# Kernel tuning notes

Measured on AMD Instinct MI355X. Metric: run time of the kernel, lower is better.

## Reference

```python
import jax, jax.numpy as jnp
import numpy as np

D = 16      # chem_dims
K = 16      # hard-coded k in Atom_embedding
N = 81920   # query points
M = 20000   # atoms
EPS = 1e-5  # BatchNorm eps


def _knn_idx(x, y, x_batch, y_batch, k, chunk=1024):
    """Block-diagonal kNN: indices of k nearest atoms in y for each point in x,
    restricted to matching batch ids (mirrors pykeops diagonal_ranges)."""
    n = x.shape[0]
    nch = n // chunk
    yb = y_batch[None, :]

    def f(args):
        xc, xbc = args                                            # [chunk,3], [chunk]
        d = jnp.sum((xc[:, None, :] - y[None, :, :]) ** 2, -1)    # [chunk, M]
        d = jnp.where(xbc[:, None] == yb, d, jnp.inf)
        _, idx = jax.lax.top_k(-d, k)                             # k smallest dists
        return idx

    idx = jax.lax.map(f, (x.reshape(nch, chunk, 3), x_batch.reshape(nch, chunk)))
    return idx.reshape(n, k)


def _bn_eval(h, gamma, beta, mean, var):
    # eval-mode BatchNorm1d over last dim
    return (h - mean) * (gamma * jax.lax.rsqrt(var + EPS)) + beta


def setup_inputs() -> dict:
    key = jax.random.key(0)
    ks = jax.random.split(key, 12)
    inp = {
        "x": jax.random.uniform(ks[0], (N, 3), jnp.float32) * 10.0,
        "y": jax.random.uniform(ks[1], (M, 3), jnp.float32) * 10.0,
        "y_atomtypes": jax.random.normal(ks[2], (M, D), jnp.float32),
        "x_batch": jnp.zeros((N,), jnp.int32),
        "y_batch": jnp.zeros((M,), jnp.int32),
        "W1": jax.random.normal(ks[3], (D + 1, D), jnp.float32) * 0.1,
        "b1": jnp.zeros((D,), jnp.float32),
        "W2": jax.random.normal(ks[4], (D, D), jnp.float32) * 0.1,
        "b2": jnp.zeros((D,), jnp.float32),
        "W3": jax.random.normal(ks[5], (2 * D, D), jnp.float32) * 0.1,
        "b3": jnp.zeros((D,), jnp.float32),
        "bn1_g": jnp.ones((D,), jnp.float32),
        "bn1_b": jnp.zeros((D,), jnp.float32),
        "bn1_m": jax.random.normal(ks[6], (D,), jnp.float32) * 0.1,
        "bn1_v": jnp.ones((D,), jnp.float32),
        "bn2_g": jnp.ones((D,), jnp.float32),
        "bn2_b": jnp.zeros((D,), jnp.float32),
        "bn2_m": jax.random.normal(ks[7], (D,), jnp.float32) * 0.1,
        "bn2_v": jnp.ones((D,), jnp.float32),
    }
    return inp


def reference(x, y, y_atomtypes, x_batch, y_batch,
              W1, b1, W2, b2, W3, b3,
              bn1_g, bn1_b, bn1_m, bn1_v,
              bn2_g, bn2_b, bn2_m, bn2_v):
    idx = _knn_idx(x, y, x_batch, y_batch, K)            # [N, K] int32
    yk = y[idx]                                          # [N, K, 3]
    dists = jnp.sum((x[:, None, :] - yk) ** 2, -1)       # [N, K]
    feat = jnp.concatenate(
        [y_atomtypes[idx], (1.0 / dists)[..., None]], -1)  # [N, K, D+1]
    # dropout in eval mode == identity
    h = feat @ W1 + b1                                   # conv1
    h = _bn_eval(jax.nn.leaky_relu(h, 0.2), bn1_g, bn1_b, bn1_m, bn1_v)
    fx1 = jnp.sum(h, axis=1)                             # [N, D]
    h2 = h @ W2 + b2                                     # conv2
    h2 = _bn_eval(jax.nn.leaky_relu(h2, 0.2), bn2_g, bn2_b, bn2_m, bn2_v)
    fx2 = jnp.sum(h2, axis=1)                            # [N, D]
    out = jnp.concatenate([fx1, fx2], -1) @ W3 + b3      # conv3 -> [N, D]
    return out
```

## Files before the change

kernel.cpp:

```cpp
#include <hip/hip_runtime.h>

#define N_PTS 81920
#define M_PTS 20000
#define NC 14
#define NCELLS 2744
#define CELLW 0.7142857143f
#define INVCELL 1.4f
#define BIGF 3.0e38f
#define CAP_STAGE 264
#define PPC 16
#define WPB 4
#define MAX_TASKS 7880

__device__ __forceinline__ int clampi(int v, int lo, int hi) {
  return v < lo ? lo : (v > hi ? hi : v);
}
__device__ __forceinline__ int cell_coord(float p) {
  return clampi((int)(p * INVCELL), 0, NC - 1);
}
__device__ __forceinline__ float floorpack(float d) {
  return __uint_as_float(__float_as_uint(d) & 0xFFFF8000u);
}


__global__ void hist_both_kernel(const float* __restrict__ y, const float* __restrict__ x,
                                 int* __restrict__ ycnt, int* __restrict__ xcnt) {
  int i = blockIdx.x * blockDim.x + threadIdx.x;
  if (i < M_PTS) {
    int c = (cell_coord(y[3*i+2])*NC + cell_coord(y[3*i+1]))*NC + cell_coord(y[3*i]);
    atomicAdd(&ycnt[c], 1);
  } else {
    int j = i - M_PTS;
    if (j < N_PTS) {
      int c = (cell_coord(x[3*j+2])*NC + cell_coord(x[3*j+1]))*NC + cell_coord(x[3*j]);
      atomicAdd(&xcnt[c], 1);
    }
  }
}

__global__ void scan2_kernel(const int* __restrict__ ycnt, int* __restrict__ ystart, int* __restrict__ ycur,
                             const int* __restrict__ xcnt, int* __restrict__ xstart, int* __restrict__ xcur,
                             int* __restrict__ tasks, int* __restrict__ ntasks) {
  const int* cnt = (blockIdx.x == 0) ? ycnt : xcnt;
  int* start     = (blockIdx.x == 0) ? ystart : xstart;
  int* cursor    = (blockIdx.x == 0) ? ycur : xcur;
  __shared__ int tmp[1024];
  int tid = threadIdx.x;
  int chunk = (NCELLS + 1023) >> 10;
  int base = tid * chunk;
  int sum = 0;
  for (int k = 0; k < chunk; ++k) {
    int j = base + k;
    if (j < NCELLS) sum += cnt[j];
  }
  tmp[tid] = sum;
  __syncthreads();
  for (int off = 1; off < 1024; off <<= 1) {
    int v = (tid >= off) ? tmp[tid - off] : 0;
    __syncthreads();
    tmp[tid] += v;
    __syncthreads();
  }
  int run = tmp[tid] - sum;
  for (int k = 0; k < chunk; ++k) {
    int j = base + k;
    if (j < NCELLS) { start[j] = run; cursor[j] = run; run += cnt[j]; }
  }
  if (tid == 1023) start[NCELLS] = tmp[1023];

  if (blockIdx.x == 1) {
    int tsum = 0;
    for (int k = 0; k < chunk; ++k) {
      int j = base + k;
      if (j < NCELLS) tsum += (cnt[j] + PPC - 1) / PPC;
    }
    __syncthreads();
    tmp[tid] = tsum;
    __syncthreads();
    for (int off = 1; off < 1024; off <<= 1) {
      int v = (tid >= off) ? tmp[tid - off] : 0;
      __syncthreads();
      tmp[tid] += v;
      __syncthreads();
    }
    int trun = tmp[tid] - tsum;
    for (int k = 0; k < chunk; ++k) {
      int j = base + k;
      if (j < NCELLS) {
        int nch = (cnt[j] + PPC - 1) / PPC;
        for (int q2 = 0; q2 < nch; ++q2) tasks[trun++] = (q2 << 12) | j;
      }
    }
    if (tid == 1023) ntasks[0] = tmp[1023];
  }
}

__global__ void scatter_both_kernel(const float* __restrict__ y, const float* __restrict__ x,
                                    int* __restrict__ ycur, int* __restrict__ xcur,
                                    float4* __restrict__ ys4, int* __restrict__ xorder,
                                    float4* __restrict__ xs4, float4* __restrict__ y4) {
  int i = blockIdx.x * blockDim.x + threadIdx.x;
  if (i < M_PTS) {
    float px = y[3*i], py = y[3*i+1], pz = y[3*i+2];
    if (y4) y4[i] = make_float4(px, py, pz, 0.0f);
    int c = (cell_coord(pz)*NC + cell_coord(py))*NC + cell_coord(px);
    int pos = atomicAdd(&ycur[c], 1);
    ys4[pos] = make_float4(px, py, pz, __int_as_float(i));
  } else {
    int j = i - M_PTS;
    if (j < N_PTS) {
      float px = x[3*j], py = x[3*j+1], pz = x[3*j+2];
      int c = (cell_coord(pz)*NC + cell_coord(py))*NC + cell_coord(px);
      int pos = atomicAdd(&xcur[c], 1);
      xorder[pos] = j;
      if (xs4) xs4[pos] = make_float4(px, py, pz, __int_as_float(j));
    }
  }
}

__global__ void sortcell_kernel(float4* __restrict__ ys4, const int* __restrict__ ystart) {
  int c = blockIdx.x * blockDim.x + threadIdx.x;
  if (c >= NCELLS) return;
  int r0 = ystart[c], r1 = ystart[c+1];
  for (int i = r0 + 1; i < r1; ++i) {
    float4 v = ys4[i];
    int key = __float_as_int(v.w);
    int j = i - 1;
    while (j >= r0 && __float_as_int(ys4[j].w) > key) { ys4[j+1] = ys4[j]; --j; }
    ys4[j+1] = v;
  }
}

__device__ __forceinline__ void bitonic_sort16(float (&d)[16]) {
  #define CE(a,b) { float lo=fminf(d[a],d[b]); float hi=fmaxf(d[a],d[b]); d[a]=lo; d[b]=hi; }
  CE(0,8) CE(1,9) CE(2,10) CE(3,11) CE(4,12) CE(5,13) CE(6,14) CE(7,15)
  CE(0,4) CE(1,5) CE(2,6) CE(3,7) CE(8,12) CE(9,13) CE(10,14) CE(11,15)
  CE(0,2) CE(1,3) CE(4,6) CE(5,7) CE(8,10) CE(9,11) CE(12,14) CE(13,15)
  CE(0,1) CE(2,3) CE(4,5) CE(6,7) CE(8,9) CE(10,11) CE(12,13) CE(14,15)
  #undef CE
}

__device__ __forceinline__ void ins16(float (&s)[16], float k) {
  #pragma unroll
  for (int j = 15; j >= 1; --j) s[j] = fminf(fmaxf(s[j-1], k), s[j]);
  s[0] = fminf(s[0], k);
}

__global__ void __launch_bounds__(256) knn_cell_kernel(
    const float4* __restrict__ xs4,
    const float4* __restrict__ ys4, const int* __restrict__ ystart,
    const int* __restrict__ xstart,
    const int* __restrict__ tasks, const int* __restrict__ ntasks,
    unsigned short* __restrict__ pi)
{
  __shared__ float4 cand_all[WPB][CAP_STAGE];
  int wid = threadIdx.x >> 6;
  int tid = threadIdx.x & 63;
  int ti = blockIdx.x * WPB + wid;
  if (ti >= ntasks[0]) return;
  int task = tasks[ti];
  int c = task & 4095, chunk = task >> 12;
  int cbeg = xstart[c];
  int cend = xstart[c+1];
  int pbeg = cbeg + chunk*PPC;
  int pend = min(cend, pbeg + PPC);

  float4* cand = cand_all[wid];

  int ccx = c % NC, ccy = (c / NC) % NC, ccz = c / (NC*NC);
  int x0 = ccx-1 < 0 ? 0 : ccx-1, x1 = ccx+1 > NC-1 ? NC-1 : ccx+1;
  int y0 = ccy-1 < 0 ? 0 : ccy-1, y1 = ccy+1 > NC-1 ? NC-1 : ccy+1;
  int z0 = ccz-1 < 0 ? 0 : ccz-1, z1 = ccz+1 > NC-1 ? NC-1 : ccz+1;

  int off = 0, nst = 0; bool ovf = false;
  for (int gz = z0; gz <= z1; ++gz) {
    for (int gy = y0; gy <= y1; ++gy) {
      int rowbase = (gz*NC + gy)*NC;
      int r0 = ystart[rowbase + x0];
      int r1 = ystart[rowbase + x1 + 1];
      int len = r1 - r0;
      if (!ovf && off + len <= CAP_STAGE) {
        for (int k = tid; k < len; k += 64) cand[off + k] = ys4[r0 + k];
        off += len; ++nst;
      } else ovf = true;
    }
  }
  int L = off;
  asm volatile("s_waitcnt vmcnt(0) lgkmcnt(0)" ::: "memory");

  int g = tid >> 2, sub = tid & 3;
  int pidx = pbeg + g;
  bool active = pidx < pend;
  int gid = active ? pidx : (pend - 1);
  float4 xq = xs4[gid];
  float xpx = xq.x, xpy = xq.y, xpz = xq.z;

  float s[16];
  #pragma unroll
  for (int j = 0; j < 16; ++j) s[j] = BIGF;

  auto packkey = [&](float4 q) -> float {
    float dx = xpx - q.x, dy = xpy - q.y, dz = xpz - q.z;
    float d = fmaf(dx, dx, fmaf(dy, dy, dz*dz));
    unsigned kb = (__float_as_uint(d) & 0xFFFF8000u) | (__float_as_uint(q.w) & 0x7FFFu);
    return __uint_as_float(kb);
  };

  auto merged16 = [&](float (&u)[16]) {
    float cb[16];
    #pragma unroll
    for (int i = 0; i < 16; ++i) cb[i] = fminf(s[i], __shfl_xor(s[15-i], 1));
    bitonic_sort16(cb);
    #pragma unroll
    for (int i = 0; i < 16; ++i) u[i] = fminf(cb[i], __shfl_xor(cb[15-i], 2));
    bitonic_sort16(u);
  };

  {
    int i = sub;
    for (; i + 4 < L; i += 8) {
      float4 q0 = cand[i], q1 = cand[i+4];
      float k0 = packkey(q0), k1 = packkey(q1);
      ins16(s, k0); ins16(s, k1);
    }
    for (; i < L; i += 4) ins16(s, packkey(cand[i]));
  }

  auto scan_row_g = [&](int xa, int xb, int rowbase) {
    int r0 = ystart[rowbase + xa];
    int r1 = ystart[rowbase + xb + 1];
    int i = r0 + sub;
    for (; i + 4 < r1; i += 8) {
      float4 q0 = ys4[i], q1 = ys4[i+4];
      float k0 = packkey(q0), k1 = packkey(q1);
      ins16(s, k0); ins16(s, k1);
    }
    for (; i < r1; i += 4) ins16(s, packkey(ys4[i]));
  };

  if (ovf) {
    int cnt2 = 0;
    for (int gz = z0; gz <= z1; ++gz)
      for (int gy = y0; gy <= y1; ++gy) {
        if (cnt2 >= nst) scan_row_g(x0, x1, (gz*NC + gy)*NC);
        ++cnt2;
      }
  }

  float u[16];
  merged16(u);
  float s15m = u[15];
  int R = 1;
  while (true) {
    float b = BIGF;
    if (ccx - R >= 0)    b = fminf(b, xpx - (float)(ccx-R)*CELLW);
    if (ccx + R <= NC-2) b = fminf(b, (float)(ccx+R+1)*CELLW - xpx);
    if (ccy - R >= 0)    b = fminf(b, xpy - (float)(ccy-R)*CELLW);
    if (ccy + R <= NC-2) b = fminf(b, (float)(ccy+R+1)*CELLW - xpy);
    if (ccz - R >= 0)    b = fminf(b, xpz - (float)(ccz-R)*CELLW);
    if (ccz + R <= NC-2) b = fminf(b, (float)(ccz+R+1)*CELLW - xpz);
    b = fmaxf(b - 1e-4f, 0.0f);
    if (s15m <= floorpack(b*b) || R >= NC) break;
    ++R;
    int z0r = ccz-R < 0 ? 0 : ccz-R, z1r = ccz+R > NC-1 ? NC-1 : ccz+R;
    int y0r = ccy-R < 0 ? 0 : ccy-R, y1r = ccy+R > NC-1 ? NC-1 : ccy+R;
    int x0r = ccx-R < 0 ? 0 : ccx-R, x1r = ccx+R > NC-1 ? NC-1 : ccx+R;
    for (int gz = z0r; gz <= z1r; ++gz) {
      int dzz = gz - ccz; if (dzz < 0) dzz = -dzz;
      float gapz = (gz > ccz) ? ((float)gz*CELLW - xpz)
                 : ((gz < ccz) ? (xpz - (float)(gz+1)*CELLW) : 0.0f);
      gapz = fmaxf(gapz - 1e-4f, 0.0f);
      float gz2 = gapz * gapz;
      for (int gy = y0r; gy <= y1r; ++gy) {
        int dyy = gy - ccy; if (dyy < 0) dyy = -dyy;
        float gapy = (gy > ccy) ? ((float)gy*CELLW - xpy)
                   : ((gy < ccy) ? (xpy - (float)(gy+1)*CELLW) : 0.0f);
        gapy = fmaxf(gapy - 1e-4f, 0.0f);
        float rowd2 = fmaf(gapy, gapy, gz2);
        if (floorpack(rowd2) >= s15m) continue;
        int rowbase = (gz*NC + gy)*NC;
        if (dzz == R || dyy == R) {
          scan_row_g(x0r, x1r, rowbase);
        } else {
          if (ccx - R >= 0) {
            float gapx = fmaxf(xpx - (float)(ccx-R+1)*CELLW - 1e-4f, 0.0f);
            if (floorpack(fmaf(gapx, gapx, rowd2)) < s15m)
              scan_row_g(ccx-R, ccx-R, rowbase);
          }
          if (ccx + R <= NC-1) {
            float gapx = fmaxf((float)(ccx+R)*CELLW - xpx - 1e-4f, 0.0f);
            if (floorpack(fmaf(gapx, gapx, rowd2)) < s15m)
              scan_row_g(ccx+R, ccx+R, rowbase);
          }
        }
      }
    }
    merged16(u);
    s15m = u[15];
  }

  if (active) {
    float v0 = u[sub*4+0], v1 = u[sub*4+1], v2 = u[sub*4+2], v3 = u[sub*4+3];
    unsigned wlo = (__float_as_uint(v0) & 0x7FFFu) | ((__float_as_uint(v1) & 0x7FFFu) << 16);
    unsigned whi = (__float_as_uint(v2) & 0x7FFFu) | ((__float_as_uint(v3) & 0x7FFFu) << 16);
    uint2 W; W.x = wlo; W.y = whi;
    ((uint2*)pi)[gid*4 + sub] = W;
  }
}

template<int CTRL>
__device__ __forceinline__ float ror_add(float v) {
  int r = __builtin_amdgcn_update_dpp(0, __float_as_int(v), CTRL, 0xF, 0xF, true);
  return v + __int_as_float(r);
}
__device__ __forceinline__ float red16(float v) {
  v = ror_add<0x121>(v);
  v = ror_add<0x122>(v);
  v = ror_add<0x124>(v);
  v = ror_add<0x128>(v);
  return v;
}

__global__ void __launch_bounds__(256) mlp_kernel(
    const float* __restrict__ yat, const float4* __restrict__ xs4, const float4* __restrict__ y4,
    const float* __restrict__ W1, const float* __restrict__ b1,
    const float* __restrict__ W2, const float* __restrict__ b2,
    const float* __restrict__ W3, const float* __restrict__ b3,
    const float* __restrict__ g1, const float* __restrict__ be1,
    const float* __restrict__ m1, const float* __restrict__ v1,
    const float* __restrict__ g2, const float* __restrict__ be2,
    const float* __restrict__ m2, const float* __restrict__ v2,
    const unsigned short* __restrict__ pi, float* __restrict__ out)
{
  int t = threadIdx.x;
  int o = t & 15;
  int gid = (blockIdx.x * 256 + t) >> 4;
  float4 xq = xs4[gid];
  int p = __float_as_int(xq.w);

  int id = (int)pi[gid*16 + o];
  float4 yq = y4[id];
  float dx = xq.x - yq.x, dy = xq.y - yq.y, dz = xq.z - yq.z;
  float dist = fmaf(dx, dx, fmaf(dy, dy, dz*dz));
  float invd = 1.0f / dist;

  const float4* a4 = (const float4*)(yat + ((size_t)id << 4));
  float4 q0 = a4[0], q1 = a4[1], q2 = a4[2], q3 = a4[3];
  float a[16];
  a[0]=q0.x; a[1]=q0.y; a[2]=q0.z; a[3]=q0.w;
  a[4]=q1.x; a[5]=q1.y; a[6]=q1.z; a[7]=q1.w;
  a[8]=q2.x; a[9]=q2.y; a[10]=q2.z; a[11]=q2.w;
  a[12]=q3.x; a[13]=q3.y; a[14]=q3.z; a[15]=q3.w;

  float h[16];
  #pragma unroll
  for (int oo = 0; oo < 16; ++oo) {
    float acc = fmaf(invd, W1[256 + oo], b1[oo]);
    #pragma unroll
    for (int i = 0; i < 16; ++i) acc = fmaf(a[i], W1[i*16 + oo], acc);
    acc = fmaxf(acc, 0.2f * acc);
    float S = g1[oo] * rsqrtf(v1[oo] + 1e-5f);
    h[oo] = fmaf(acc - m1[oo], S, be1[oo]);
  }

  float f2[16];
  #pragma unroll
  for (int oo = 0; oo < 16; ++oo) {
    float acc = b2[oo];
    #pragma unroll
    for (int i = 0; i < 16; ++i) acc = fmaf(h[i], W2[i*16 + oo], acc);
    acc = fmaxf(acc, 0.2f * acc);
    float S = g2[oo] * rsqrtf(v2[oo] + 1e-5f);
    f2[oo] = fmaf(acc - m2[oo], S, be2[oo]);
  }

  float acc = b3[o];
  #pragma unroll
  for (int i = 0; i < 16; ++i) acc = fmaf(red16(h[i]),  W3[i*16 + o], acc);
  #pragma unroll
  for (int i = 0; i < 16; ++i) acc = fmaf(red16(f2[i]), W3[(16 + i)*16 + o], acc);

  out[(size_t)p*16 + o] = acc;
}

__device__ __forceinline__ void stage_weights(float* lds, int t,
    const float* W1, const float* b1, const float* W2, const float* b2,
    const float* W3, const float* b3,
    const float* g1, const float* be1, const float* m1, const float* v1,
    const float* g2, const float* be2, const float* m2, const float* v2)
{
  for (int k = t; k < 272; k += 256) { int i = k >> 4, o = k & 15; lds[o*20 + i] = W1[k]; }
  for (int k = t; k < 256; k += 256) { int i = k >> 4, o = k & 15; lds[320 + o*16 + i] = W2[k]; }
  for (int k = t; k < 512; k += 256) { int i = k >> 4, o = k & 15; lds[576 + o*32 + i] = W3[k]; }
  if (t < 16) {
    lds[1088 + t] = b1[t];
    lds[1104 + t] = b2[t];
    lds[1120 + t] = b3[t];
    float s1 = g1[t] * rsqrtf(v1[t] + 1e-5f);
    lds[1136 + t] = s1;
    lds[1152 + t] = be1[t] - m1[t]*s1;
    float s2 = g2[t] * rsqrtf(v2[t] + 1e-5f);
    lds[1168 + t] = s2;
    lds[1184 + t] = be2[t] - m2[t]*s2;
  }
}

__device__ __forceinline__ void topk_insert(float (&s)[16], int (&si)[16], float d, int qi) {
  #pragma unroll
  for (int j = 15; j >= 1; --j) {
    bool c1 = d < s[j-1];
    bool c2 = d < s[j];
    float ns = c1 ? s[j-1] : (c2 ? d : s[j]);
    int  ni = c1 ? si[j-1] : (c2 ? qi : si[j]);
    s[j] = ns; si[j] = ni;
  }
  if (d < s[0]) { si[0] = qi; s[0] = d; }
}

__device__ __forceinline__ void mlp_and_store(const float* lds, const float2* spill, int t,
    const float* __restrict__ yat, float* __restrict__ out, int p)
{
  const float* W1t = lds;
  const float* W2t = lds + 320;
  const float* W3t = lds + 576;
  const float* sb1 = lds + 1088;
  const float* sb2 = lds + 1104;
  const float* sb3 = lds + 1120;
  const float* S1 = lds + 1136;
  const float* T1 = lds + 1152;
  const float* S2 = lds + 1168;
  const float* T2 = lds + 1184;

  float fx1[16], fx2[16];
  #pragma unroll
  for (int o = 0; o < 16; ++o) { fx1[o] = 0.0f; fx2[o] = 0.0f; }

  #pragma unroll 1
  for (int j = 0; j < 16; ++j) {
    float2 sv = spill[j*256 + t];
    float invd = 1.0f / sv.x;
    int id = __float_as_int(sv.y);
    const float4* a4 = (const float4*)(yat + ((size_t)id << 4));
    float4 q0 = a4[0], q1 = a4[1], q2 = a4[2], q3 = a4[3];
    float a[16];
    a[0]=q0.x; a[1]=q0.y; a[2]=q0.z; a[3]=q0.w;
    a[4]=q1.x; a[5]=q1.y; a[6]=q1.z; a[7]=q1.w;
    a[8]=q2.x; a[9]=q2.y; a[10]=q2.z; a[11]=q2.w;
    a[12]=q3.x; a[13]=q3.y; a[14]=q3.z; a[15]=q3.w;
    float h[16];
    #pragma unroll
    for (int o = 0; o < 16; ++o) {
      float acc = fmaf(invd, W1t[o*20 + 16], sb1[o]);
      #pragma unroll
      for (int i = 0; i < 16; ++i) acc = fmaf(a[i], W1t[o*20 + i], acc);
      acc = fmaxf(acc, 0.2f * acc);
      float hv = fmaf(acc, S1[o], T1[o]);
      h[o] = hv;
      fx1[o] += hv;
    }
    #pragma unroll
    for (int o = 0; o < 16; ++o) {
      float acc = sb2[o];
      #pragma unroll
      for (int i = 0; i < 16; ++i) acc = fmaf(h[i], W2t[o*16 + i], acc);
      acc = fmaxf(acc, 0.2f * acc);
      fx2[o] += fmaf(acc, S2[o], T2[o]);
    }
  }

  float res[16];
  #pragma unroll
  for (int o = 0; o < 16; ++o) {
    float acc = sb3[o];
    #pragma unroll
    for (int i = 0; i < 16; ++i) acc = fmaf(fx1[i], W3t[o*32 + i], acc);
    #pragma unroll
    for (int i = 0; i < 16; ++i) acc = fmaf(fx2[i], W3t[o*32 + 16 + i], acc);
    res[o] = acc;
  }
  float* op = out + ((size_t)p << 4);
  float4 r;
  r.x=res[0]; r.y=res[1]; r.z=res[2]; r.w=res[3];   ((float4*)op)[0] = r;
  r.x=res[4]; r.y=res[5]; r.z=res[6]; r.w=res[7];   ((float4*)op)[1] = r;
  r.x=res[8]; r.y=res[9]; r.z=res[10]; r.w=res[11]; ((float4*)op)[2] = r;
  r.x=res[12]; r.y=res[13]; r.z=res[14]; r.w=res[15];((float4*)op)[3] = r;
}

__global__ void __launch_bounds__(256) knn_mlp_fused_kernel(
    const float* __restrict__ x, const float* __restrict__ yat,
    const float* __restrict__ W1, const float* __restrict__ b1,
    const float* __restrict__ W2, const float* __restrict__ b2,
    const float* __restrict__ W3, const float* __restrict__ b3,
    const float* __restrict__ g1, const float* __restrict__ be1,
    const float* __restrict__ m1, const float* __restrict__ v1,
    const float* __restrict__ g2, const float* __restrict__ be2,
    const float* __restrict__ m2, const float* __restrict__ v2,
    const float4* __restrict__ ys4, const int* __restrict__ ystart,
    const int* __restrict__ xorder, float* __restrict__ out)
{
  __shared__ float lds[1200];
  __shared__ float2 spill[4096];
  int t = threadIdx.x;
  stage_weights(lds, t, W1,b1,W2,b2,W3,b3, g1,be1,m1,v1, g2,be2,m2,v2);
  __syncthreads();

  int gid = blockIdx.x * 256 + t;
  int p = xorder[gid];
  float xpx = x[3*p], xpy = x[3*p+1], xpz = x[3*p+2];
  int cx = cell_coord(xpx), cy = cell_coord(xpy), cz = cell_coord(xpz);

  float s[16]; int si[16];
  #pragma unroll
  for (int j = 0; j < 16; ++j) { s[j] = BIGF; si[j] = 0; }

  auto scan_row = [&](int gz, int gy, int xa, int xb) {
    int rowbase = (gz*NC + gy)*NC;
    int r0 = ystart[rowbase + xa];
    int r1 = ystart[rowbase + xb + 1];
    for (int i = r0; i < r1; ++i) {
      float4 q = ys4[i];
      float dx = xpx - q.x, dy = xpy - q.y, dz = xpz - q.z;
      float d = fmaf(dx, dx, fmaf(dy, dy, dz*dz));
      if (d < s[15]) topk_insert(s, si, d, __float_as_int(q.w));
    }
  };

  {
    int z0 = cz-1 < 0 ? 0 : cz-1, z1 = cz+1 > NC-1 ? NC-1 : cz+1;
    int y0 = cy-1 < 0 ? 0 : cy-1, y1 = cy+1 > NC-1 ? NC-1 : cy+1;
    int x0 = cx-1 < 0 ? 0 : cx-1, x1 = cx+1 > NC-1 ? NC-1 : cx+1;
    for (int gz = z0; gz <= z1; ++gz)
      for (int gy = y0; gy <= y1; ++gy)
        scan_row(gz, gy, x0, x1);
  }

  int R = 1;
  while (true) {
    float b = BIGF;
    if (cx - R >= 0)    b = fminf(b, xpx - (float)(cx-R)*CELLW);
    if (cx + R <= NC-2) b = fminf(b, (float)(cx+R+1)*CELLW - xpx);
    if (cy - R >= 0)    b = fminf(b, xpy - (float)(cy-R)*CELLW);
    if (cy + R <= NC-2) b = fminf(b, (float)(cy+R+1)*CELLW - xpy);
    if (cz - R >= 0)    b = fminf(b, xpz - (float)(cz-R)*CELLW);
    if (cz + R <= NC-2) b = fminf(b, (float)(cz+R+1)*CELLW - xpz);
    b = fmaxf(b - 1e-4f, 0.0f);
    if (s[15] <= b*b || R >= NC) break;
    ++R;
    int z0 = cz-R < 0 ? 0 : cz-R, z1 = cz+R > NC-1 ? NC-1 : cz+R;
    int y0 = cy-R < 0 ? 0 : cy-R, y1 = cy+R > NC-1 ? NC-1 : cy+R;
    int x0 = cx-R < 0 ? 0 : cx-R, x1 = cx+R > NC-1 ? NC-1 : cx+R;
    for (int gz = z0; gz <= z1; ++gz) {
      int dzz = gz - cz; if (dzz < 0) dzz = -dzz;
      for (int gy = y0; gy <= y1; ++gy) {
        int dyy = gy - cy; if (dyy < 0) dyy = -dyy;
        if (dzz == R || dyy == R) {
          scan_row(gz, gy, x0, x1);
        } else {
          if (cx - R >= 0)    scan_row(gz, gy, cx-R, cx-R);
          if (cx + R <= NC-1) scan_row(gz, gy, cx+R, cx+R);
        }
      }
    }
  }

  #pragma unroll
  for (int j = 0; j < 16; ++j) spill[j*256 + t] = make_float2(s[j], __int_as_float(si[j]));
  mlp_and_store(lds, spill, t, yat, out, p);
}

__global__ void __launch_bounds__(256) brute_kernel(
    const float* __restrict__ x, const float* __restrict__ y, const float* __restrict__ yat,
    const float* __restrict__ W1, const float* __restrict__ b1,
    const float* __restrict__ W2, const float* __restrict__ b2,
    const float* __restrict__ W3, const float* __restrict__ b3,
    const float* __restrict__ g1, const float* __restrict__ be1,
    const float* __restrict__ m1, const float* __restrict__ v1,
    const float* __restrict__ g2, const float* __restrict__ be2,
    const float* __restrict__ m2, const float* __restrict__ v2,
    float* __restrict__ out)
{
  __shared__ float lds[1200];
  __shared__ float2 spill[4096];
  __shared__ float4 ybuf[1024];
  int t = threadIdx.x;
  stage_weights(lds, t, W1,b1,W2,b2,W3,b3, g1,be1,m1,v1, g2,be2,m2,v2);

  int gid = blockIdx.x * 256 + t;
  float xpx = x[3*gid], xpy = x[3*gid+1], xpz = x[3*gid+2];
  float s[16]; int si[16];
  #pragma unroll
  for (int j = 0; j < 16; ++j) { s[j] = BIGF; si[j] = 0; }

  for (int base = 0; base < M_PTS; base += 1024) {
    int nload = M_PTS - base; if (nload > 1024) nload = 1024;
    __syncthreads();
    for (int k = t; k < nload; k += 256) {
      int i = base + k;
      ybuf[k] = make_float4(y[3*i], y[3*i+1], y[3*i+2], __int_as_float(i));
    }
    __syncthreads();
    for (int i2 = 0; i2 < nload; ++i2) {
      float4 q = ybuf[i2];
      float dx = xpx - q.x, dy = xpy - q.y, dz = xpz - q.z;
      float d = fmaf(dx, dx, fmaf(dy, dy, dz*dz));
      if (d < s[15]) topk_insert(s, si, d, __float_as_int(q.w));
    }
  }

  #pragma unroll
  for (int j = 0; j < 16; ++j) spill[j*256 + t] = make_float2(s[j], __int_as_float(si[j]));
  mlp_and_store(lds, spill, t, yat, out, gid);
}

extern "C" void kernel_launch(void* const* d_in, const int* in_sizes, int n_in,
                              void* d_out, int out_size, void* d_ws, size_t ws_size,
                              hipStream_t stream) {
  const float* x   = (const float*)d_in[0];
  const float* y   = (const float*)d_in[1];
  const float* yat = (const float*)d_in[2];
  const float* W1  = (const float*)d_in[5];
  const float* b1  = (const float*)d_in[6];
  const float* W2  = (const float*)d_in[7];
  const float* b2  = (const float*)d_in[8];
  const float* W3  = (const float*)d_in[9];
  const float* b3  = (const float*)d_in[10];
  const float* g1  = (const float*)d_in[11];
  const float* be1 = (const float*)d_in[12];
  const float* m1  = (const float*)d_in[13];
  const float* v1  = (const float*)d_in[14];
  const float* g2  = (const float*)d_in[15];
  const float* be2 = (const float*)d_in[16];
  const float* m2  = (const float*)d_in[17];
  const float* v2  = (const float*)d_in[18];
  float* out = (float*)d_out;

  const size_t WS_SPLIT = 4997424;
  const size_t WS_FUSED = 760000;

  if (ws_size >= WS_SPLIT) {
    char* ws = (char*)d_ws;
    float4* ys4 = (float4*)(ws);
    float4* y4  = (float4*)(ws + 320000);
    float4* xs4 = (float4*)(ws + 640000);
    int* xorder = (int*)(ws + 1950720);
    unsigned short* pi = (unsigned short*)(ws + 2278400);
    int* ycnt   = (int*)(ws + 4899840);
    int* xcnt   = (int*)(ws + 4910848);
    int* ystart = (int*)(ws + 4921856);
    int* ycur   = (int*)(ws + 4932864);
    int* xstart = (int*)(ws + 4943872);
    int* xcur   = (int*)(ws + 4954880);
    int* ntasks = (int*)(ws + 4965888);
    int* tasks  = (int*)(ws + 4965904);

    hipMemsetAsync(ws + 4899840, 0, 22016, stream);
    int grid_mn = (M_PTS + N_PTS + 255) / 256;
    hist_both_kernel<<<grid_mn, 256, 0, stream>>>(y, x, ycnt, xcnt);
    scan2_kernel<<<2, 1024, 0, stream>>>(ycnt, ystart, ycur, xcnt, xstart, xcur,
                                         tasks, ntasks);
    scatter_both_kernel<<<grid_mn, 256, 0, stream>>>(y, x, ycur, xcur, ys4, xorder, xs4, y4);
    knn_cell_kernel<<<MAX_TASKS/WPB, 256, 0, stream>>>(xs4, ys4, ystart, xstart,
        tasks, ntasks, pi);
    mlp_kernel<<<(N_PTS*16)/256, 256, 0, stream>>>(yat, xs4, y4, W1,b1,W2,b2,W3,b3,
        g1,be1,m1,v1, g2,be2,m2,v2, pi, out);
  } else if (ws_size >= WS_FUSED) {
    char* ws = (char*)d_ws;
    float4* ys4 = (float4*)(ws);
    int* xorder = (int*)(ws + 320000);
    int* ycnt   = (int*)(ws + 647680);
    int* xcnt   = (int*)(ws + 658688);
    int* ystart = (int*)(ws + 669696);
    int* ycur   = (int*)(ws + 680704);
    int* xstart = (int*)(ws + 691712);
    int* xcur   = (int*)(ws + 702720);
    int* tasks  = (int*)(ws + 713728);
    int* ntasks = (int*)(ws + 713728);

    hipMemsetAsync(ws + 647680, 0, 22016, stream);
    int grid_mn = (M_PTS + N_PTS + 255) / 256;
    hist_both_kernel<<<grid_mn, 256, 0, stream>>>(y, x, ycnt, xcnt);
    scan2_kernel<<<2, 1024, 0, stream>>>(ycnt, ystart, ycur, xcnt, xstart, xcur,
                                         tasks + 4, ntasks);
    scatter_both_kernel<<<grid_mn, 256, 0, stream>>>(y, x, ycur, xcur, ys4, xorder, nullptr, nullptr);
    sortcell_kernel<<<(NCELLS+255)/256, 256, 0, stream>>>(ys4, ystart);
    knn_mlp_fused_kernel<<<N_PTS/256, 256, 0, stream>>>(x, yat, W1,b1,W2,b2,W3,b3,
        g1,be1,m1,v1, g2,be2,m2,v2, ys4, ystart, xorder, out);
  } else {
    brute_kernel<<<N_PTS/256, 256, 0, stream>>>(x, y, yat, W1,b1,W2,b2,W3,b3,
        g1,be1,m1,v1, g2,be2,m2,v2, out);
  }
}
```

Baseline: 115.3 us.

## Precompute per-cell neighbor row offsets and stage candidates with one flat loop

Adds a cellinfo kernel that precomputes, for each cell, the 9 neighbor-row start offsets and their cumulative lengths, packed into 16 ints. The kNN kernel loads this with four int4 reads and fills the shared candidate buffer in a single flat loop, replacing nine serial row loops that each read ystart. Overflow beyond the staging capacity now goes through the same mapping instead of rescanning whole rows. The task index is also made wave-uniform with readfirstlane. The cost is an extra kernel launch, more workspace, and some per-element select arithmetic to map each index back to its row.

```diff
diff --git a/kernel.cpp b/kernel.cpp
--- a/kernel.cpp
+++ b/kernel.cpp
@@ -93,6 +93,34 @@
     }
     if (tid == 1023) ntasks[0] = tmp[1023];
   }
+}
+
+__global__ void cellinfo_kernel(const int* __restrict__ ystart, int* __restrict__ cinfo) {
+  int c = blockIdx.x * blockDim.x + threadIdx.x;
+  if (c >= NCELLS) return;
+  int ccx = c % NC, ccy = (c / NC) % NC, ccz = c / (NC*NC);
+  int x0 = ccx-1 < 0 ? 0 : ccx-1, x1 = ccx+1 > NC-1 ? NC-1 : ccx+1;
+  int y0 = ccy-1 < 0 ? 0 : ccy-1, y1 = ccy+1 > NC-1 ? NC-1 : ccy+1;
+  int z0 = ccz-1 < 0 ? 0 : ccz-1, z1 = ccz+1 > NC-1 ? NC-1 : ccz+1;
+  int r0s[9]; int cums[10]; cums[0] = 0; int nr = 0;
+  for (int gz = z0; gz <= z1; ++gz)
+    for (int gy = y0; gy <= y1; ++gy) {
+      int rowbase = (gz*NC + gy)*NC;
+      int r0 = ystart[rowbase + x0];
+      int len = ystart[rowbase + x1 + 1] - r0;
+      r0s[nr] = r0; cums[nr+1] = cums[nr] + len; ++nr;
+    }
+  for (int j = nr; j < 9; ++j) { r0s[j] = 0; cums[j+1] = cums[j]; }
+  int* o = cinfo + c*16;
+  #pragma unroll
+  for (int j = 0; j < 9; ++j) o[j] = r0s[j];
+  o[9]  = cums[1] | (cums[2] << 16);
+  o[10] = cums[3] | (cums[4] << 16);
+  o[11] = cums[5] | (cums[6] << 16);
+  o[12] = cums[7] | (cums[8] << 16);
+  o[13] = cums[9];
+  o[14] = cums[9];
+  o[15] = 0;
 }
 
 __global__ void scatter_both_kernel(const float* __restrict__ y, const float* __restrict__ x,
@@ -151,6 +179,7 @@
     const float4* __restrict__ ys4, const int* __restrict__ ystart,
     const int* __restrict__ xstart,
     const int* __restrict__ tasks, const int* __restrict__ ntasks,
+    const int* __restrict__ cinfo,
     unsigned short* __restrict__ pi)
 {
   __shared__ float4 cand_all[WPB][CAP_STAGE];
@@ -158,7 +187,7 @@
   int tid = threadIdx.x & 63;
   int ti = blockIdx.x * WPB + wid;
   if (ti >= ntasks[0]) return;
-  int task = tasks[ti];
+  int task = __builtin_amdgcn_readfirstlane(tasks[ti]);
   int c = task & 4095, chunk = task >> 12;
   int cbeg = xstart[c];
   int cend = xstart[c+1];
@@ -168,24 +197,35 @@
   float4* cand = cand_all[wid];
 
   int ccx = c % NC, ccy = (c / NC) % NC, ccz = c / (NC*NC);
-  int x0 = ccx-1 < 0 ? 0 : ccx-1, x1 = ccx+1 > NC-1 ? NC-1 : ccx+1;
-  int y0 = ccy-1 < 0 ? 0 : ccy-1, y1 = ccy+1 > NC-1 ? NC-1 : ccy+1;
-  int z0 = ccz-1 < 0 ? 0 : ccz-1, z1 = ccz+1 > NC-1 ? NC-1 : ccz+1;
-
-  int off = 0, nst = 0; bool ovf = false;
-  for (int gz = z0; gz <= z1; ++gz) {
-    for (int gy = y0; gy <= y1; ++gy) {
-      int rowbase = (gz*NC + gy)*NC;
-      int r0 = ystart[rowbase + x0];
-      int r1 = ystart[rowbase + x1 + 1];
-      int len = r1 - r0;
-      if (!ovf && off + len <= CAP_STAGE) {
-        for (int k = tid; k < len; k += 64) cand[off + k] = ys4[r0 + k];
-        off += len; ++nst;
-      } else ovf = true;
-    }
-  }
-  int L = off;
+
+  const int4* ci = (const int4*)(cinfo + (size_t)c*16);
+  int4 ca = ci[0], cb = ci[1], cc2 = ci[2], cd = ci[3];
+  int r0a = ca.x, r0b = ca.y, r0c = ca.z, r0d = ca.w;
+  int r0e = cb.x, r0f = cb.y, r0g = cb.z, r0h = cb.w, r0i = cc2.x;
+  int cum1 = cc2.y & 0xFFFF, cum2 = ((unsigned)cc2.y) >> 16;
+  int cum3 = cc2.z & 0xFFFF, cum4 = ((unsigned)cc2.z) >> 16;
+  int cum5 = cc2.w & 0xFFFF, cum6 = ((unsigned)cc2.w) >> 16;
+  int cum7 = cd.x & 0xFFFF, cum8 = ((unsigned)cd.x) >> 16;
+  int cum9 = cd.y;
+  int L = cd.z;
+
+  auto region_addr = [&](int k) -> int {
+    int row = (k >= cum1) + (k >= cum2) + (k >= cum3) + (k >= cum4) +
+              (k >= cum5) + (k >= cum6) + (k >= cum7) + (k >= cum8) + (k >= cum9);
+    int base = r0a, st = 0;
+    base = (row == 1) ? r0b : base; st = (row == 1) ? cum1 : st;
+    base = (row == 2) ? r0c : base; st = (row == 2) ? cum2 : st;
+    base = (row == 3) ? r0d : base; st = (row == 3) ? cum3 : st;
+    base = (row == 4) ? r0e : base; st = (row == 4) ? cum4 : st;
+    base = (row == 5) ? r0f : base; st = (row == 5) ? cum5 : st;
+    base = (row == 6) ? r0g : base; st = (row == 6) ? cum6 : st;
+    base = (row == 7) ? r0h : base; st = (row == 7) ? cum7 : st;
+    base = (row == 8) ? r0i : base; st = (row == 8) ? cum8 : st;
+    return base + (k - st);
+  };
+
+  int Ls = L < CAP_STAGE ? L : CAP_STAGE;
+  for (int k = tid; k < Ls; k += 64) cand[k] = ys4[region_addr(k)];
   asm volatile("s_waitcnt vmcnt(0) lgkmcnt(0)" ::: "memory");
 
   int g = tid >> 2, sub = tid & 3;
@@ -207,23 +247,25 @@
   };
 
   auto merged16 = [&](float (&u)[16]) {
-    float cb[16];
+    float cbf[16];
     #pragma unroll
-    for (int i = 0; i < 16; ++i) cb[i] = fminf(s[i], __shfl_xor(s[15-i], 1));
-    bitonic_sort16(cb);
+    for (int i = 0; i < 16; ++i) cbf[i] = fminf(s[i], __shfl_xor(s[15-i], 1));
+    bitonic_sort16(cbf);
     #pragma unroll
-    for (int i = 0; i < 16; ++i) u[i] = fminf(cb[i], __shfl_xor(cb[15-i], 2));
+    for (int i = 0; i < 16; ++i) u[i] = fminf(cbf[i], __shfl_xor(cbf[15-i], 2));
     bitonic_sort16(u);
   };
 
   {
     int i = sub;
-    for (; i + 4 < L; i += 8) {
+    for (; i + 4 < Ls; i += 8) {
       float4 q0 = cand[i], q1 = cand[i+4];
       float k0 = packkey(q0), k1 = packkey(q1);
       ins16(s, k0); ins16(s, k1);
     }
-    for (; i < L; i += 4) ins16(s, packkey(cand[i]));
+    for (; i < Ls; i += 4) ins16(s, packkey(cand[i]));
+    for (int k2 = CAP_STAGE + sub; k2 < L; k2 += 4)
+      ins16(s, packkey(ys4[region_addr(k2)]));
   }
 
   auto scan_row_g = [&](int xa, int xb, int rowbase) {
@@ -237,15 +279,6 @@
     }
     for (; i < r1; i += 4) ins16(s, packkey(ys4[i]));
   };
-
-  if (ovf) {
-    int cnt2 = 0;
-    for (int gz = z0; gz <= z1; ++gz)
-      for (int gy = y0; gy <= y1; ++gy) {
-        if (cnt2 >= nst) scan_row_g(x0, x1, (gz*NC + gy)*NC);
-        ++cnt2;
-      }
-  }
 
   float u[16];
   merged16(u);
@@ -634,7 +667,7 @@
   const float* v2  = (const float*)d_in[18];
   float* out = (float*)d_out;
 
-  const size_t WS_SPLIT = 4997424;
+  const size_t WS_SPLIT = 5173040;
   const size_t WS_FUSED = 760000;
 
   if (ws_size >= WS_SPLIT) {
@@ -652,15 +685,17 @@
     int* xcur   = (int*)(ws + 4954880);
     int* ntasks = (int*)(ws + 4965888);
     int* tasks  = (int*)(ws + 4965904);
+    int* cinfo  = (int*)(ws + 4997424);
 
     hipMemsetAsync(ws + 4899840, 0, 22016, stream);
     int grid_mn = (M_PTS + N_PTS + 255) / 256;
     hist_both_kernel<<<grid_mn, 256, 0, stream>>>(y, x, ycnt, xcnt);
     scan2_kernel<<<2, 1024, 0, stream>>>(ycnt, ystart, ycur, xcnt, xstart, xcur,
                                          tasks, ntasks);
+    cellinfo_kernel<<<(NCELLS+255)/256, 256, 0, stream>>>(ystart, cinfo);
     scatter_both_kernel<<<grid_mn, 256, 0, stream>>>(y, x, ycur, xcur, ys4, xorder, xs4, y4);
     knn_cell_kernel<<<MAX_TASKS/WPB, 256, 0, stream>>>(xs4, ys4, ystart, xstart,
-        tasks, ntasks, pi);
+        tasks, ntasks, cinfo, pi);
     mlp_kernel<<<(N_PTS*16)/256, 256, 0, stream>>>(yat, xs4, y4, W1,b1,W2,b2,W3,b3,
         g1,be1,m1,v1, g2,be2,m2,v2, pi, out);
   } else if (ws_size >= WS_FUSED) {
```

After: 132.2 us. 14.6% more time.
